# Performance work log

Measured on AMD Instinct MI355X. Metric: run time of the kernel, lower is better.

Reference implementation:

```python
import jax, jax.numpy as jnp
import numpy as np

NUM_HEADS = 8
HEAD_DIM = 64  # output_size
HIDDEN = 512
N_NODES = 4096


def setup_inputs() -> dict:
    key = jax.random.key(0)
    ks = jax.random.split(key, 9)
    s = 0.02
    return {
        "x": jax.random.normal(ks[0], (N_NODES, HIDDEN), dtype=jnp.float32),
        "Wq_w": jax.random.normal(ks[1], (HIDDEN, NUM_HEADS * HEAD_DIM), dtype=jnp.float32) * s,
        "Wq_b": jax.random.normal(ks[2], (NUM_HEADS * HEAD_DIM,), dtype=jnp.float32) * s,
        "Wk_w": jax.random.normal(ks[3], (HIDDEN, NUM_HEADS * HEAD_DIM), dtype=jnp.float32) * s,
        "Wk_b": jax.random.normal(ks[4], (NUM_HEADS * HEAD_DIM,), dtype=jnp.float32) * s,
        "Wv_w": jax.random.normal(ks[5], (HIDDEN, NUM_HEADS * HEAD_DIM), dtype=jnp.float32) * s,
        "Wv_b": jax.random.normal(ks[6], (NUM_HEADS * HEAD_DIM,), dtype=jnp.float32) * s,
        "Wo_w": jax.random.normal(ks[7], (NUM_HEADS * HEAD_DIM, HEAD_DIM), dtype=jnp.float32) * s,
        "Wo_b": jax.random.normal(ks[8], (HEAD_DIM,), dtype=jnp.float32) * s,
    }


def reference(x, Wq_w, Wq_b, Wk_w, Wk_b, Wv_w, Wv_b, Wo_w, Wo_b):
    N = x.shape[0]
    H, d = NUM_HEADS, HEAD_DIM
    # Projections: [N, H*d] -> [H, N, d]
    q = (x @ Wq_w + Wq_b).reshape(N, H, d).transpose(1, 0, 2)
    k = (x @ Wk_w + Wk_b).reshape(N, H, d).transpose(1, 0, 2)
    v = (x @ Wv_w + Wv_b).reshape(N, H, d).transpose(1, 0, 2)
    # Scaled dot-product attention per head: [H, N, N]
    scores = jnp.einsum('hnd,hmd->hnm', q, k) / jnp.sqrt(jnp.float32(d))
    attention_weights = jax.nn.softmax(scores, axis=-1)
    attended = jnp.einsum('hnm,hmd->hnd', attention_weights, v)  # [H, N, d]
    attended = attended.transpose(1, 0, 2).reshape(N, H * d)
    output = attended @ Wo_w + Wo_b  # [N, d]
    return output, attention_weights
```

## Files before the change

### kernel.cpp

```cpp
#include <hip/hip_runtime.h>

#define NN 4096
#define HID 512
#define NH 8
#define HD 64

typedef __attribute__((ext_vector_type(8))) short short8;
typedef __attribute__((ext_vector_type(4))) float f32x4;

__device__ __forceinline__ ushort f2bf(float f) {
    unsigned u = __float_as_uint(f);
    return (ushort)((u + 0x7FFFu + ((u >> 16) & 1u)) >> 16);
}

__device__ __forceinline__ void gld16(const void* g, void* l) {
    __builtin_amdgcn_global_load_lds(
        (const __attribute__((address_space(1))) void*)g,
        (__attribute__((address_space(3))) void*)l, 16, 0, 0);
}

__global__ __launch_bounds__(256) void qkv_kernel(
    const float* __restrict__ x,
    const float* __restrict__ Wq, const float* __restrict__ bq,
    const float* __restrict__ Wk, const float* __restrict__ bk,
    const float* __restrict__ Wv, const float* __restrict__ bv,
    ushort* __restrict__ Qb, char* __restrict__ Kbs, char* __restrict__ Vts)
{
    const int mat = blockIdx.z;
    const float* W = (mat == 0) ? Wq : ((mat == 1) ? Wk : Wv);
    const float* b = (mat == 0) ? bq : ((mat == 1) ? bk : bv);

    const int row0 = blockIdx.y * 128;
    const int col0 = blockIdx.x * 64;
    const int tid = threadIdx.x;
    const int tx = tid & 15, ty = tid >> 4;

    __shared__ float xs[32][132];
    __shared__ float wt[32][68];
    __shared__ __align__(16) ushort vts[64][136];

    float acc[8][4];
#pragma unroll
    for (int i = 0; i < 8; ++i)
#pragma unroll
        for (int j = 0; j < 4; ++j) acc[i][j] = 0.f;

    for (int kc = 0; kc < HID; kc += 32) {
#pragma unroll
        for (int it = 0; it < 4; ++it) {
            int f = it * 256 + tid;
            int i = f >> 3, k4 = f & 7;
            float4 v = *(const float4*)(x + (size_t)(row0 + i) * HID + kc + k4 * 4);
            xs[k4 * 4 + 0][i] = v.x; xs[k4 * 4 + 1][i] = v.y;
            xs[k4 * 4 + 2][i] = v.z; xs[k4 * 4 + 3][i] = v.w;
        }
#pragma unroll
        for (int it = 0; it < 2; ++it) {
            int f = it * 256 + tid;
            int k = f >> 4, c4 = f & 15;
            float4 v = *(const float4*)(W + (size_t)(kc + k) * HID + col0 + c4 * 4);
            *(float4*)&wt[k][c4 * 4] = v;
        }
        __syncthreads();
        for (int k = 0; k < 32; ++k) {
            float a0[8], b0[4];
            *(float4*)&a0[0] = *(const float4*)&xs[k][ty * 4];
            *(float4*)&a0[4] = *(const float4*)&xs[k][64 + ty * 4];
            *(float4*)&b0[0] = *(const float4*)&wt[k][tx * 4];
#pragma unroll
            for (int i = 0; i < 8; ++i)
#pragma unroll
                for (int j = 0; j < 4; ++j)
                    acc[i][j] = fmaf(a0[i], b0[j], acc[i][j]);
        }
        __syncthreads();
    }

    const int head = col0 >> 6;
    if (mat == 0) {
#pragma unroll
        for (int bi = 0; bi < 2; ++bi)
#pragma unroll
            for (int ii = 0; ii < 4; ++ii) {
                int r = row0 + bi * 64 + ty * 4 + ii;
                ushort4 u;
                u.x = f2bf(acc[bi * 4 + ii][0] + b[col0 + tx * 4 + 0]);
                u.y = f2bf(acc[bi * 4 + ii][1] + b[col0 + tx * 4 + 1]);
                u.z = f2bf(acc[bi * 4 + ii][2] + b[col0 + tx * 4 + 2]);
                u.w = f2bf(acc[bi * 4 + ii][3] + b[col0 + tx * 4 + 3]);
                *(ushort4*)(Qb + ((size_t)head * NN + r) * HD + tx * 4) = u;
            }
    } else if (mat == 1) {
#pragma unroll
        for (int bi = 0; bi < 2; ++bi)
#pragma unroll
            for (int ii = 0; ii < 4; ++ii) {
                int r = row0 + bi * 64 + ty * 4 + ii;
                ushort4 u;
                u.x = f2bf(acc[bi * 4 + ii][0] + b[col0 + tx * 4 + 0]);
                u.y = f2bf(acc[bi * 4 + ii][1] + b[col0 + tx * 4 + 1]);
                u.z = f2bf(acc[bi * 4 + ii][2] + b[col0 + tx * 4 + 2]);
                u.w = f2bf(acc[bi * 4 + ii][3] + b[col0 + tx * 4 + 3]);
                int bc = (tx * 8) ^ ((r & 7) << 4);
                *(ushort4*)(Kbs + ((size_t)head * NN + r) * 128 + bc) = u;
            }
    } else {
#pragma unroll
        for (int bi = 0; bi < 2; ++bi)
#pragma unroll
            for (int ii = 0; ii < 4; ++ii) {
                int rl = bi * 64 + ty * 4 + ii;
#pragma unroll
                for (int j = 0; j < 4; ++j) {
                    int cl = tx * 4 + j;
                    vts[cl][rl] = f2bf(acc[bi * 4 + ii][j] + b[col0 + cl]);
                }
            }
        __syncthreads();
        int cl = tid >> 2, q = tid & 3;
        int dsw = (cl & 7) << 4;
        char* dstrow = Vts + (size_t)(col0 + cl) * NN * 2;
        int colb0 = (row0 + q * 32) * 2;
#pragma unroll
        for (int k8 = 0; k8 < 4; ++k8)
            *(uint4*)(dstrow + ((colb0 + k8 * 16) ^ dsw)) =
                *(const uint4*)(&vts[cl][q * 32 + k8 * 8]);
    }
}

__global__ __launch_bounds__(512, 4) void attn_kernel(
    const ushort* __restrict__ Qb, const char* __restrict__ Kbs,
    const char* __restrict__ Vts,
    float* __restrict__ wout, float* __restrict__ att)
{
    const int h = blockIdx.x & 7;
    const int row0 = ((blockIdx.x >> 3) + (blockIdx.y << 3)) * 64;
    const int tid = threadIdx.x;
    const int w = tid >> 6, lane = tid & 63;
    const int g = lane >> 4, li = lane & 15;
    const int rgrp = w >> 1, khalf = w & 1;
    const int qr = row0 + rgrp * 16;

    const ushort* Qh = Qb + (size_t)h * NN * HD;
    const char* Kh = Kbs + (size_t)h * NN * 128;
    const char* Vh = Vts + (size_t)h * HD * NN * 2;
    float* WH = wout + ((size_t)h << 24);

    __shared__ __align__(16) char smem[81920];
    char* kbuf0 = smem;
    char* kbuf1 = smem + 16384;
    char* vbuf0 = smem + 32768;
    char* vbuf1 = smem + 49152;
    char* pbuf  = smem + 65536;
    float* zpart = (float*)(smem + 65536);
    float* attstage = (float*)(smem + 65536);

    const short8 qa0 = *(const short8*)(Qh + (size_t)(qr + li) * HD + g * 8);
    const short8 qa1 = *(const short8*)(Qh + (size_t)(qr + li) * HD + 32 + g * 8);
    const int sw = (li & 7) << 4;

    const int kl0 = w * 16 + (lane >> 3);
    const int kbase0 = (kl0 & 63) + ((kl0 >= 64) ? 2048 : 0);
    const int kl1 = kl0 + 8;
    const int kbase1 = (kl1 & 63) + ((kl1 >= 64) ? 2048 : 0);
    const size_t koff0 = (size_t)kbase0 * 128 + (lane & 7) * 16;
    const size_t koff1 = (size_t)kbase1 * 128 + (lane & 7) * 16;
    const int vd0 = w * 8 + (lane >> 4);
    const int vd1 = vd0 + 4;
    const size_t voff0 = (size_t)vd0 * 8192 + ((lane >> 3) & 1) * 4096 + (lane & 7) * 16;
    const size_t voff1 = (size_t)vd1 * 8192 + ((lane >> 3) & 1) * 4096 + (lane & 7) * 16;
    const int ldst = w * 2048 + lane * 16;

    float zsum = 0.f;
    gld16(Kh + koff0, kbuf0 + ldst);
    gld16(Kh + koff1 + 0, kbuf0 + ldst + 1024);
    __syncthreads();
    {
        char* kb_cur = kbuf0; char* kb_nxt = kbuf1;
        for (int t = 0; t < 32; ++t) {
            if (t < 31) {
                gld16(Kh + (size_t)(t + 1) * 8192 + koff0, kb_nxt + ldst);
                gld16(Kh + (size_t)(t + 1) * 8192 + koff1, kb_nxt + ldst + 1024);
            }
#pragma unroll
            for (int jt = 0; jt < 4; ++jt) {
                const char* rp = kb_cur + (khalf * 64 + jt * 16 + li) * 128;
                short8 kb0 = *(const short8*)(rp + ((g * 16) ^ sw));
                short8 kb1 = *(const short8*)(rp + ((64 + g * 16) ^ sw));
                f32x4 acc = {0.f, 0.f, 0.f, 0.f};
                acc = __builtin_amdgcn_mfma_f32_16x16x32_bf16(kb0, qa0, acc, 0, 0, 0);
                acc = __builtin_amdgcn_mfma_f32_16x16x32_bf16(kb1, qa1, acc, 0, 0, 0);
#pragma unroll
                for (int r = 0; r < 4; ++r) zsum += __expf(acc[r] * 0.125f);
            }
            __syncthreads();
            char* tmp = kb_cur; kb_cur = kb_nxt; kb_nxt = tmp;
        }
    }
    zsum += __shfl_xor(zsum, 16);
    zsum += __shfl_xor(zsum, 32);
    if (lane < 16) zpart[w * 16 + li] = zsum;
    __syncthreads();
    const float iz = 1.0f / (zpart[(rgrp * 2) * 16 + li] + zpart[(rgrp * 2 + 1) * 16 + li]);
    __syncthreads();

    f32x4 pv[4];
#pragma unroll
    for (int dt = 0; dt < 4; ++dt) pv[dt] = (f32x4){0.f, 0.f, 0.f, 0.f};
    char* myp = pbuf + w * 2048;

    gld16(Kh + koff0, kbuf0 + ldst);
    gld16(Kh + koff1, kbuf0 + ldst + 1024);
    gld16(Vh + voff0, vbuf0 + ldst);
    gld16(Vh + voff1, vbuf0 + ldst + 1024);
    __syncthreads();
    {
        char* kb_cur = kbuf0; char* kb_nxt = kbuf1;
        char* vb_cur = vbuf0; char* vb_nxt = vbuf1;
        for (int t = 0; t < 32; ++t) {
            if (t < 31) {
                gld16(Kh + (size_t)(t + 1) * 8192 + koff0, kb_nxt + ldst);
                gld16(Kh + (size_t)(t + 1) * 8192 + koff1, kb_nxt + ldst + 1024);
                gld16(Vh + (size_t)(t + 1) * 128 + voff0, vb_nxt + ldst);
                gld16(Vh + (size_t)(t + 1) * 128 + voff1, vb_nxt + ldst + 1024);
            }
#pragma unroll
            for (int jt = 0; jt < 4; ++jt) {
                const char* rp = kb_cur + (khalf * 64 + jt * 16 + li) * 128;
                short8 kb0 = *(const short8*)(rp + ((g * 16) ^ sw));
                short8 kb1 = *(const short8*)(rp + ((64 + g * 16) ^ sw));
                f32x4 acc = {0.f, 0.f, 0.f, 0.f};
                acc = __builtin_amdgcn_mfma_f32_16x16x32_bf16(kb0, qa0, acc, 0, 0, 0);
                acc = __builtin_amdgcn_mfma_f32_16x16x32_bf16(kb1, qa1, acc, 0, 0, 0);
                f32x4 ev;
#pragma unroll
                for (int r = 0; r < 4; ++r) ev[r] = __expf(acc[r] * 0.125f) * iz;
                *(f32x4*)(WH + (size_t)(qr + li) * NN + khalf * 2048 + t * 64 + jt * 16 + g * 4) = ev;
                uint pk0 = (uint)f2bf(ev[0]) | ((uint)f2bf(ev[1]) << 16);
                uint pk1 = (uint)f2bf(ev[2]) | ((uint)f2bf(ev[3]) << 16);
                int boff = (li * 128 + jt * 32 + g * 8) ^ sw;
                *(uint2*)(myp + boff) = make_uint2(pk0, pk1);
            }
#pragma unroll
            for (int kb2 = 0; kb2 < 2; ++kb2) {
                int rbp = (li * 128 + kb2 * 64 + g * 16) ^ sw;
                short8 pa = *(const short8*)(myp + rbp);
#pragma unroll
                for (int dt = 0; dt < 4; ++dt) {
                    const char* vrp = vb_cur + (dt * 16 + li) * 256 + khalf * 128;
                    short8 vbf = *(const short8*)(vrp + ((kb2 * 64 + g * 16) ^ sw));
                    pv[dt] = __builtin_amdgcn_mfma_f32_16x16x32_bf16(pa, vbf, pv[dt], 0, 0, 0);
                }
            }
            __syncthreads();
            char* tmp = kb_cur; kb_cur = kb_nxt; kb_nxt = tmp;
            tmp = vb_cur; vb_cur = vb_nxt; vb_nxt = tmp;
        }
    }

    if (khalf == 1) {
#pragma unroll
        for (int dt = 0; dt < 4; ++dt)
#pragma unroll
            for (int r = 0; r < 4; ++r)
                attstage[(rgrp * 16 + g * 4 + r) * 64 + dt * 16 + li] = pv[dt][r];
    }
    __syncthreads();
    if (khalf == 0) {
#pragma unroll
        for (int dt = 0; dt < 4; ++dt)
#pragma unroll
            for (int r = 0; r < 4; ++r) {
                float v = pv[dt][r] + attstage[(rgrp * 16 + g * 4 + r) * 64 + dt * 16 + li];
                att[(size_t)(qr + g * 4 + r) * HID + h * HD + dt * 16 + li] = v;
            }
    }
}

__global__ __launch_bounds__(256) void out_kernel(
    const float* __restrict__ att, const float* __restrict__ Wo,
    const float* __restrict__ bo, float* __restrict__ outp)
{
    const int row0 = blockIdx.x * 16;
    const int tid = threadIdx.x;
    const int tx = tid & 15, ty = tid >> 4;

    __shared__ float as_[64][20];
    __shared__ float ws2[64][68];

    float acc[4] = {0.f, 0.f, 0.f, 0.f};

    for (int kc = 0; kc < HID; kc += 64) {
        {
            int i = tid >> 4, k4 = tid & 15;
            float4 v = *(const float4*)(att + (size_t)(row0 + i) * HID + kc + k4 * 4);
            as_[k4 * 4 + 0][i] = v.x; as_[k4 * 4 + 1][i] = v.y;
            as_[k4 * 4 + 2][i] = v.z; as_[k4 * 4 + 3][i] = v.w;
        }
#pragma unroll
        for (int it = 0; it < 4; ++it) {
            int f = it * 256 + tid;
            int k = f >> 4, c4 = f & 15;
            float4 v = *(const float4*)(Wo + (size_t)(kc + k) * HD + c4 * 4);
            *(float4*)&ws2[k][c4 * 4] = v;
        }
        __syncthreads();
        for (int k = 0; k < 64; ++k) {
            float a = as_[k][ty];
            float4 b0 = *(const float4*)&ws2[k][tx * 4];
            acc[0] = fmaf(a, b0.x, acc[0]);
            acc[1] = fmaf(a, b0.y, acc[1]);
            acc[2] = fmaf(a, b0.z, acc[2]);
            acc[3] = fmaf(a, b0.w, acc[3]);
        }
        __syncthreads();
    }

    float4 v;
    v.x = acc[0] + bo[tx * 4 + 0];
    v.y = acc[1] + bo[tx * 4 + 1];
    v.z = acc[2] + bo[tx * 4 + 2];
    v.w = acc[3] + bo[tx * 4 + 3];
    *(float4*)(outp + (size_t)(row0 + ty) * HD + tx * 4) = v;
}

extern "C" void kernel_launch(void* const* d_in, const int* in_sizes, int n_in,
                              void* d_out, int out_size, void* d_ws, size_t ws_size,
                              hipStream_t stream) {
    const float* x  = (const float*)d_in[0];
    const float* Wq = (const float*)d_in[1];
    const float* bq = (const float*)d_in[2];
    const float* Wk = (const float*)d_in[3];
    const float* bk = (const float*)d_in[4];
    const float* Wv = (const float*)d_in[5];
    const float* bv = (const float*)d_in[6];
    const float* Wo = (const float*)d_in[7];
    const float* bo = (const float*)d_in[8];

    float* out  = (float*)d_out;
    float* wout = out + (size_t)NN * HD;

    char* wsb = (char*)d_ws;
    ushort* Qb  = (ushort*)wsb;
    char*   Kbs = wsb + 4u * 1024u * 1024u;
    char*   Vts = wsb + 8u * 1024u * 1024u;
    float*  att = (float*)(wsb + 12u * 1024u * 1024u);

    hipLaunchKernelGGL(qkv_kernel, dim3(8, 32, 3), dim3(256), 0, stream,
                       x, Wq, bq, Wk, bk, Wv, bv, Qb, Kbs, Vts);
    hipLaunchKernelGGL(attn_kernel, dim3(64, NH), dim3(512), 0, stream,
                       Qb, Kbs, Vts, wout, att);
    hipLaunchKernelGGL(out_kernel, dim3(256), dim3(256), 0, stream,
                       att, Wo, bo, out);
}
```

Measured before the change: 294.5 us.

## Pipeline K/V LDS loads with explicit vmcnt waits and one barrier per tile

Replaces the two __syncthreads per tile iteration with a single s_barrier at the top of each iteration. Explicit s_waitcnt vmcnt values let only the current tile's global-to-LDS loads be waited on while later prefetches stay in flight. The first (normalizer) pass becomes triple-buffered, reusing vbuf0 as a third K buffer to prefetch two tiles ahead. Both passes aim to cut barrier stalls and hide more global-load latency. Correctness now depends on hand-counted vmcnt values, and the attention-weight global stores in the second loop also count toward vmcnt.

Measured after the change: 278.3 us. 1.06x faster.

```diff
diff --git a/kernel.cpp b/kernel.cpp
--- a/kernel.cpp
+++ b/kernel.cpp
@@ -172,19 +172,25 @@
     const int ldst = w * 2048 + lane * 16;
 
     float zsum = 0.f;
-    gld16(Kh + koff0, kbuf0 + ldst);
-    gld16(Kh + koff1 + 0, kbuf0 + ldst + 1024);
-    __syncthreads();
     {
-        char* kb_cur = kbuf0; char* kb_nxt = kbuf1;
+        char* c0 = kbuf0; char* c1 = kbuf1; char* c2 = vbuf0;
+        gld16(Kh + koff0, c0 + ldst);
+        gld16(Kh + koff1, c0 + ldst + 1024);
+        gld16(Kh + 8192 + koff0, c1 + ldst);
+        gld16(Kh + 8192 + koff1, c1 + ldst + 1024);
+        asm volatile("" ::: "memory");
         for (int t = 0; t < 32; ++t) {
-            if (t < 31) {
-                gld16(Kh + (size_t)(t + 1) * 8192 + koff0, kb_nxt + ldst);
-                gld16(Kh + (size_t)(t + 1) * 8192 + koff1, kb_nxt + ldst + 1024);
-            }
+            if (t < 31) { asm volatile("s_waitcnt vmcnt(2)" ::: "memory"); }
+            else        { asm volatile("s_waitcnt vmcnt(0)" ::: "memory"); }
+            __builtin_amdgcn_s_barrier();
+            if (t + 2 < 32) {
+                gld16(Kh + (size_t)(t + 2) * 8192 + koff0, c2 + ldst);
+                gld16(Kh + (size_t)(t + 2) * 8192 + koff1, c2 + ldst + 1024);
+            }
+            asm volatile("" ::: "memory");
 #pragma unroll
             for (int jt = 0; jt < 4; ++jt) {
-                const char* rp = kb_cur + (khalf * 64 + jt * 16 + li) * 128;
+                const char* rp = c0 + (khalf * 64 + jt * 16 + li) * 128;
                 short8 kb0 = *(const short8*)(rp + ((g * 16) ^ sw));
                 short8 kb1 = *(const short8*)(rp + ((64 + g * 16) ^ sw));
                 f32x4 acc = {0.f, 0.f, 0.f, 0.f};
@@ -193,8 +199,7 @@
 #pragma unroll
                 for (int r = 0; r < 4; ++r) zsum += __expf(acc[r] * 0.125f);
             }
-            __syncthreads();
-            char* tmp = kb_cur; kb_cur = kb_nxt; kb_nxt = tmp;
+            char* tmp = c0; c0 = c1; c1 = c2; c2 = tmp;
         }
     }
     zsum += __shfl_xor(zsum, 16);
@@ -209,24 +214,28 @@
     for (int dt = 0; dt < 4; ++dt) pv[dt] = (f32x4){0.f, 0.f, 0.f, 0.f};
     char* myp = pbuf + w * 2048;
 
-    gld16(Kh + koff0, kbuf0 + ldst);
-    gld16(Kh + koff1, kbuf0 + ldst + 1024);
-    gld16(Vh + voff0, vbuf0 + ldst);
-    gld16(Vh + voff1, vbuf0 + ldst + 1024);
-    __syncthreads();
     {
-        char* kb_cur = kbuf0; char* kb_nxt = kbuf1;
-        char* vb_cur = vbuf0; char* vb_nxt = vbuf1;
+        char* kc = kbuf0; char* kn = kbuf1;
+        char* vc = vbuf0; char* vn = vbuf1;
+        gld16(Kh + koff0, kc + ldst);
+        gld16(Kh + koff1, kc + ldst + 1024);
+        gld16(Vh + voff0, vc + ldst);
+        gld16(Vh + voff1, vc + ldst + 1024);
+        asm volatile("" ::: "memory");
         for (int t = 0; t < 32; ++t) {
-            if (t < 31) {
-                gld16(Kh + (size_t)(t + 1) * 8192 + koff0, kb_nxt + ldst);
-                gld16(Kh + (size_t)(t + 1) * 8192 + koff1, kb_nxt + ldst + 1024);
-                gld16(Vh + (size_t)(t + 1) * 128 + voff0, vb_nxt + ldst);
-                gld16(Vh + (size_t)(t + 1) * 128 + voff1, vb_nxt + ldst + 1024);
-            }
+            if (t == 0) { asm volatile("s_waitcnt vmcnt(0)" ::: "memory"); }
+            else        { asm volatile("s_waitcnt vmcnt(4)" ::: "memory"); }
+            __builtin_amdgcn_s_barrier();
+            if (t + 1 < 32) {
+                gld16(Kh + (size_t)(t + 1) * 8192 + koff0, kn + ldst);
+                gld16(Kh + (size_t)(t + 1) * 8192 + koff1, kn + ldst + 1024);
+                gld16(Vh + (size_t)(t + 1) * 128 + voff0, vn + ldst);
+                gld16(Vh + (size_t)(t + 1) * 128 + voff1, vn + ldst + 1024);
+            }
+            asm volatile("" ::: "memory");
 #pragma unroll
             for (int jt = 0; jt < 4; ++jt) {
-                const char* rp = kb_cur + (khalf * 64 + jt * 16 + li) * 128;
+                const char* rp = kc + (khalf * 64 + jt * 16 + li) * 128;
                 short8 kb0 = *(const short8*)(rp + ((g * 16) ^ sw));
                 short8 kb1 = *(const short8*)(rp + ((64 + g * 16) ^ sw));
                 f32x4 acc = {0.f, 0.f, 0.f, 0.f};
@@ -247,17 +256,17 @@
                 short8 pa = *(const short8*)(myp + rbp);
 #pragma unroll
                 for (int dt = 0; dt < 4; ++dt) {
-                    const char* vrp = vb_cur + (dt * 16 + li) * 256 + khalf * 128;
+                    const char* vrp = vc + (dt * 16 + li) * 256 + khalf * 128;
                     short8 vbf = *(const short8*)(vrp + ((kb2 * 64 + g * 16) ^ sw));
                     pv[dt] = __builtin_amdgcn_mfma_f32_16x16x32_bf16(pa, vbf, pv[dt], 0, 0, 0);
                 }
             }
-            __syncthreads();
-            char* tmp = kb_cur; kb_cur = kb_nxt; kb_nxt = tmp;
-            tmp = vb_cur; vb_cur = vb_nxt; vb_nxt = tmp;
-        }
-    }
-
+            char* tmp = kc; kc = kn; kn = tmp;
+            tmp = vc; vc = vn; vn = tmp;
+        }
+    }
+
+    __syncthreads();
     if (khalf == 1) {
 #pragma unroll
         for (int dt = 0; dt < 4; ++dt)
```
